# Performance work log

Measured on AMD Instinct MI355X. Metric: run time of the kernel, lower is better.

Reference implementation:

```python
import jax, jax.numpy as jnp
import numpy as np

EPS = 1e-12  # torch F.normalize eps

def _normalize(x):
    # L2-normalize along last dim, matching F.normalize(dim=-1)
    n = jnp.linalg.norm(x, axis=-1, keepdims=True)
    return x / jnp.maximum(n, EPS)

def setup_inputs() -> dict:
    key = jax.random.key(0)
    k1, k2, k3 = jax.random.split(key, 3)
    B, K, D = 32768, 8, 256
    return {
        "drone_slots": jax.random.normal(k1, (B, K, D), dtype=jnp.float32),
        "sat_slots": jax.random.normal(k2, (B, K, D), dtype=jnp.float32),
        "labels": jax.random.randint(k3, (B,), 0, 1000, dtype=jnp.int64),
        "temperature": 0.1,
    }

def reference(drone_slots, sat_slots, labels, temperature):
    # labels are unused by the original math (targets are arange(K))
    ds = _normalize(drone_slots)  # [B,K,D]
    ss = _normalize(sat_slots)    # [B,K,D]
    logits = jnp.einsum("bkd,bjd->bkj", ds, ss) / temperature  # [B,K,K]
    # cross_entropy with targets = arange(K): positive is the diagonal
    lse = jax.nn.logsumexp(logits, axis=-1)                      # [B,K]
    pos = jnp.diagonal(logits, axis1=-2, axis2=-1)               # [B,K]
    ce_per_sample = jnp.mean(lse - pos, axis=-1)                 # [B], per-sample mean-reduced CE
    return jnp.mean(ce_per_sample)                               # average over batch
```

## Files before the change

kernel.cpp:

```cpp
#include <hip/hip_runtime.h>


#define GSTAGE(P, NH) do {                                              \
    const unsigned bp = (lane >> (P)) & 1u;                             \
    _Pragma("unroll")                                                   \
    for (int c = 0; c < (NH); ++c) {                                    \
      float keep = bp ? g[(NH) + c] : g[c];                             \
      float send = bp ? g[c] : g[(NH) + c];                             \
      g[c] = keep + __shfl_xor(send, 1 << (P), 64);                     \
    }                                                                   \
  } while (0)

#define NSTAGE(arr, LB, NH, MASK) do {                                  \
    const unsigned bp = (lane >> (LB)) & 1u;                            \
    _Pragma("unroll")                                                   \
    for (int c = 0; c < (NH); ++c) {                                    \
      float keep = bp ? arr[(NH) + c] : arr[c];                         \
      float send = bp ? arr[c] : arr[(NH) + c];                         \
      arr[c] = keep + __shfl_xor(send, (MASK), 64);                     \
    }                                                                   \
  } while (0)

extern "C" __global__ __launch_bounds__(256, 2)
void slot_ce_main(const float* __restrict__ ds, const float* __restrict__ ss,
                  const float* __restrict__ tptr, float* __restrict__ ws,
                  int B, int nwaves) {
  const int tid  = blockIdx.x * blockDim.x + threadIdx.x;
  const int wave = tid >> 6;
  const int lane = threadIdx.x & 63;
  const float inv_t = 1.0f / tptr[0];

  float acc = 0.0f;

  for (int b = wave; b < B; b += nwaves) {
    const float4* av = (const float4*)(ds + (size_t)b * 2048);
    const float4* sv = (const float4*)(ss + (size_t)b * 2048);
    float4 A[8], S[8];
#pragma unroll
    for (int k = 0; k < 8; ++k) {
      A[k] = av[k * 64 + lane];
      S[k] = sv[k * 64 + lane];
    }

    float g[64];
#pragma unroll
    for (int k = 0; k < 8; ++k)
#pragma unroll
      for (int j = 0; j < 8; ++j)
        g[k * 8 + j] = A[k].x * S[j].x + A[k].y * S[j].y +
                       A[k].z * S[j].z + A[k].w * S[j].w;

    float na[8], nb[8];
#pragma unroll
    for (int k = 0; k < 8; ++k) {
      na[k] = A[k].x * A[k].x + A[k].y * A[k].y + A[k].z * A[k].z + A[k].w * A[k].w;
      nb[k] = S[k].x * S[k].x + S[k].y * S[k].y + S[k].z * S[k].z + S[k].w * S[k].w;
    }

    GSTAGE(5, 32); GSTAGE(4, 16); GSTAGE(3, 8);
    GSTAGE(2, 4);  GSTAGE(1, 2);  GSTAGE(0, 1);

    NSTAGE(na, 5, 4, 32); NSTAGE(na, 4, 2, 16); NSTAGE(na, 3, 1, 8);
    na[0] += __shfl_xor(na[0], 4, 64);
    na[0] += __shfl_xor(na[0], 2, 64);
    na[0] += __shfl_xor(na[0], 1, 64);
    NSTAGE(nb, 2, 4, 4); NSTAGE(nb, 1, 2, 2); NSTAGE(nb, 0, 1, 1);
    nb[0] += __shfl_xor(nb[0], 32, 64);
    nb[0] += __shfl_xor(nb[0], 16, 64);
    nb[0] += __shfl_xor(nb[0],  8, 64);

    float logit = g[0] * rsqrtf(na[0] * nb[0]) * inv_t;

    float m = logit;
    m = fmaxf(m, __shfl_xor(m, 1, 64));
    m = fmaxf(m, __shfl_xor(m, 2, 64));
    m = fmaxf(m, __shfl_xor(m, 4, 64));
    float e = __expf(logit - m);
    e += __shfl_xor(e, 1, 64);
    e += __shfl_xor(e, 2, 64);
    e += __shfl_xor(e, 4, 64);
    float lse = m + __logf(e);

    acc += lse * 0.125f;
    if ((lane >> 3) == (lane & 7)) acc -= logit;
  }

  __shared__ float red[4];
#pragma unroll
  for (int o = 32; o >= 1; o >>= 1) acc += __shfl_xor(acc, o, 64);
  if (lane == 0) red[threadIdx.x >> 6] = acc;
  __syncthreads();
  if (threadIdx.x == 0)
    ws[blockIdx.x] = (red[0] + red[1]) + (red[2] + red[3]);
}

extern "C" __global__ __launch_bounds__(256)
void slot_ce_finish(const float* __restrict__ ws, float* __restrict__ out,
                    int nparts, float scale) {
  __shared__ float red[256];
  float s = 0.0f;
  for (int i = threadIdx.x; i < nparts; i += 256) s += ws[i];
  red[threadIdx.x] = s;
  __syncthreads();
  for (int o = 128; o >= 1; o >>= 1) {
    if ((int)threadIdx.x < o) red[threadIdx.x] += red[threadIdx.x + o];
    __syncthreads();
  }
  if (threadIdx.x == 0) out[0] = red[0] * scale;
}

extern "C" void kernel_launch(void* const* d_in, const int* in_sizes, int n_in,
                              void* d_out, int out_size, void* d_ws, size_t ws_size,
                              hipStream_t stream) {
  const float* ds   = (const float*)d_in[0];
  const float* ss   = (const float*)d_in[1];
  const float* tptr = (const float*)d_in[3];
  float* out = (float*)d_out;
  float* ws  = (float*)d_ws;

  const int B = in_sizes[0] / (8 * 256);
  const int blocks = 2048;
  const int nwaves = blocks * (256 / 64);

  slot_ce_main<<<blocks, 256, 0, stream>>>(ds, ss, tptr, ws, B, nwaves);
  const float scale = 1.0f / (8.0f * (float)B);
  slot_ce_finish<<<1, 256, 0, stream>>>(ws, out, blocks, scale);
}
```

Before: 99.38 us.

## Compute slot similarity with bf16 MFMA over two-sample tiles per wave

Replaces the per-sample FP32 dot products and butterfly shuffle reductions with a 16x16x32 bf16 MFMA. Each wave handles two batch samples (16 rows) at once and keeps only the diagonal 8x8 blocks of the result. Launch changes from a persistent grid-stride loop to one tile per wave. The inputs are converted to bf16 for the matmul while the norms stay in FP32, which loses precision and needs extra conversion ALU work. The kernel also assumes B is even.

```diff
diff --git a/kernel.cpp b/kernel.cpp
--- a/kernel.cpp
+++ b/kernel.cpp
@@ -1,94 +1,91 @@
 #include <hip/hip_runtime.h>
 
 
-#define GSTAGE(P, NH) do {                                              \
-    const unsigned bp = (lane >> (P)) & 1u;                             \
-    _Pragma("unroll")                                                   \
-    for (int c = 0; c < (NH); ++c) {                                    \
-      float keep = bp ? g[(NH) + c] : g[c];                             \
-      float send = bp ? g[c] : g[(NH) + c];                             \
-      g[c] = keep + __shfl_xor(send, 1 << (P), 64);                     \
-    }                                                                   \
-  } while (0)
+typedef __attribute__((ext_vector_type(8))) short bf16x8;
+typedef __attribute__((ext_vector_type(4))) float f32x4;
 
-#define NSTAGE(arr, LB, NH, MASK) do {                                  \
-    const unsigned bp = (lane >> (LB)) & 1u;                            \
-    _Pragma("unroll")                                                   \
-    for (int c = 0; c < (NH); ++c) {                                    \
-      float keep = bp ? arr[(NH) + c] : arr[c];                         \
-      float send = bp ? arr[c] : arr[(NH) + c];                         \
-      arr[c] = keep + __shfl_xor(send, (MASK), 64);                     \
-    }                                                                   \
-  } while (0)
+__device__ inline short f2bf(float f) {
+  union { float f; unsigned u; } v; v.f = f;
+  unsigned u = v.u;
+  u += 0x7fffu + ((u >> 16) & 1u);
+  return (short)(u >> 16);
+}
 
-extern "C" __global__ __launch_bounds__(256, 2)
-void slot_ce_main(const float* __restrict__ ds, const float* __restrict__ ss,
+extern "C" __global__ __launch_bounds__(256)
+void slot_ce_mfma(const float* __restrict__ ds, const float* __restrict__ ss,
                   const float* __restrict__ tptr, float* __restrict__ ws,
-                  int B, int nwaves) {
-  const int tid  = blockIdx.x * blockDim.x + threadIdx.x;
-  const int wave = tid >> 6;
+                  int ntiles) {
   const int lane = threadIdx.x & 63;
+  const int wid  = (blockIdx.x * (blockDim.x >> 6)) + (threadIdx.x >> 6);
+  const int m = lane & 15;
+  const int h = lane >> 4;
   const float inv_t = 1.0f / tptr[0];
 
-  float acc = 0.0f;
+  float loss = 0.0f;
 
-  for (int b = wave; b < B; b += nwaves) {
-    const float4* av = (const float4*)(ds + (size_t)b * 2048);
-    const float4* sv = (const float4*)(ss + (size_t)b * 2048);
-    float4 A[8], S[8];
+  if (wid < ntiles) {
+    const float4* pa = (const float4*)(ds + (size_t)wid * 4096);
+    const float4* pb = (const float4*)(ss + (size_t)wid * 4096);
+    const int base = m * 64 + h * 2;
+
+    f32x4 acc = {0.f, 0.f, 0.f, 0.f};
+    float ssqA = 0.f, ssqS = 0.f;
+
 #pragma unroll
-    for (int k = 0; k < 8; ++k) {
-      A[k] = av[k * 64 + lane];
-      S[k] = sv[k * 64 + lane];
+    for (int kb = 0; kb < 8; ++kb) {
+      const int idx = base + kb * 8;
+      float4 a0 = pa[idx], a1 = pa[idx + 1];
+      float4 s0 = pb[idx], s1 = pb[idx + 1];
+
+      ssqA += a0.x*a0.x + a0.y*a0.y + a0.z*a0.z + a0.w*a0.w
+            + a1.x*a1.x + a1.y*a1.y + a1.z*a1.z + a1.w*a1.w;
+      ssqS += s0.x*s0.x + s0.y*s0.y + s0.z*s0.z + s0.w*s0.w
+            + s1.x*s1.x + s1.y*s1.y + s1.z*s1.z + s1.w*s1.w;
+
+      bf16x8 af = { f2bf(a0.x), f2bf(a0.y), f2bf(a0.z), f2bf(a0.w),
+                    f2bf(a1.x), f2bf(a1.y), f2bf(a1.z), f2bf(a1.w) };
+      bf16x8 sf = { f2bf(s0.x), f2bf(s0.y), f2bf(s0.z), f2bf(s0.w),
+                    f2bf(s1.x), f2bf(s1.y), f2bf(s1.z), f2bf(s1.w) };
+      acc = __builtin_amdgcn_mfma_f32_16x16x32_bf16(af, sf, acc, 0, 0, 0);
     }
 
-    float g[64];
+    ssqA += __shfl_xor(ssqA, 16, 64);
+    ssqA += __shfl_xor(ssqA, 32, 64);
+    ssqS += __shfl_xor(ssqS, 16, 64);
+    ssqS += __shfl_xor(ssqS, 32, 64);
+    float na0 = __shfl(ssqA, h * 4 + 0, 64);
+    float na1 = __shfl(ssqA, h * 4 + 1, 64);
+    float na2 = __shfl(ssqA, h * 4 + 2, 64);
+    float na3 = __shfl(ssqA, h * 4 + 3, 64);
+
+    float lg0 = acc[0] * rsqrtf(na0 * ssqS) * inv_t;
+    float lg1 = acc[1] * rsqrtf(na1 * ssqS) * inv_t;
+    float lg2 = acc[2] * rsqrtf(na2 * ssqS) * inv_t;
+    float lg3 = acc[3] * rsqrtf(na3 * ssqS) * inv_t;
+
+    float c = 0.0f;
 #pragma unroll
-    for (int k = 0; k < 8; ++k)
-#pragma unroll
-      for (int j = 0; j < 8; ++j)
-        g[k * 8 + j] = A[k].x * S[j].x + A[k].y * S[j].y +
-                       A[k].z * S[j].z + A[k].w * S[j].w;
-
-    float na[8], nb[8];
-#pragma unroll
-    for (int k = 0; k < 8; ++k) {
-      na[k] = A[k].x * A[k].x + A[k].y * A[k].y + A[k].z * A[k].z + A[k].w * A[k].w;
-      nb[k] = S[k].x * S[k].x + S[k].y * S[k].y + S[k].z * S[k].z + S[k].w * S[k].w;
+    for (int r = 0; r < 4; ++r) {
+      float lg = r == 0 ? lg0 : r == 1 ? lg1 : r == 2 ? lg2 : lg3;
+      float mx = lg;
+      mx = fmaxf(mx, __shfl_xor(mx, 1, 64));
+      mx = fmaxf(mx, __shfl_xor(mx, 2, 64));
+      mx = fmaxf(mx, __shfl_xor(mx, 4, 64));
+      float e = __expf(lg - mx);
+      e += __shfl_xor(e, 1, 64);
+      e += __shfl_xor(e, 2, 64);
+      e += __shfl_xor(e, 4, 64);
+      float lse = mx + __logf(e);
+      c += lse * 0.125f;
+      if (4 * h + r == m) c -= lg;
     }
-
-    GSTAGE(5, 32); GSTAGE(4, 16); GSTAGE(3, 8);
-    GSTAGE(2, 4);  GSTAGE(1, 2);  GSTAGE(0, 1);
-
-    NSTAGE(na, 5, 4, 32); NSTAGE(na, 4, 2, 16); NSTAGE(na, 3, 1, 8);
-    na[0] += __shfl_xor(na[0], 4, 64);
-    na[0] += __shfl_xor(na[0], 2, 64);
-    na[0] += __shfl_xor(na[0], 1, 64);
-    NSTAGE(nb, 2, 4, 4); NSTAGE(nb, 1, 2, 2); NSTAGE(nb, 0, 1, 1);
-    nb[0] += __shfl_xor(nb[0], 32, 64);
-    nb[0] += __shfl_xor(nb[0], 16, 64);
-    nb[0] += __shfl_xor(nb[0],  8, 64);
-
-    float logit = g[0] * rsqrtf(na[0] * nb[0]) * inv_t;
-
-    float m = logit;
-    m = fmaxf(m, __shfl_xor(m, 1, 64));
-    m = fmaxf(m, __shfl_xor(m, 2, 64));
-    m = fmaxf(m, __shfl_xor(m, 4, 64));
-    float e = __expf(logit - m);
-    e += __shfl_xor(e, 1, 64);
-    e += __shfl_xor(e, 2, 64);
-    e += __shfl_xor(e, 4, 64);
-    float lse = m + __logf(e);
-
-    acc += lse * 0.125f;
-    if ((lane >> 3) == (lane & 7)) acc -= logit;
+    if ((m >= 8) == (h >= 2)) loss = c;
   }
 
+#pragma unroll
+  for (int o = 32; o >= 1; o >>= 1) loss += __shfl_xor(loss, o, 64);
   __shared__ float red[4];
-#pragma unroll
-  for (int o = 32; o >= 1; o >>= 1) acc += __shfl_xor(acc, o, 64);
-  if (lane == 0) red[threadIdx.x >> 6] = acc;
+  if (lane == 0) red[threadIdx.x >> 6] = loss;
   __syncthreads();
   if (threadIdx.x == 0)
     ws[blockIdx.x] = (red[0] + red[1]) + (red[2] + red[3]);
@@ -118,11 +115,11 @@
   float* out = (float*)d_out;
   float* ws  = (float*)d_ws;
 
-  const int B = in_sizes[0] / (8 * 256);
-  const int blocks = 2048;
-  const int nwaves = blocks * (256 / 64);
+  const int B      = in_sizes[0] / (8 * 256);
+  const int ntiles = B / 2;
+  const int blocks = (ntiles + 3) / 4;
 
-  slot_ce_main<<<blocks, 256, 0, stream>>>(ds, ss, tptr, ws, B, nwaves);
+  slot_ce_mfma<<<blocks, 256, 0, stream>>>(ds, ss, tptr, ws, ntiles);
   const float scale = 1.0f / (8.0f * (float)B);
   slot_ce_finish<<<1, 256, 0, stream>>>(ws, out, blocks, scale);
 }
```

Result: slower. 106.6 us (+7.2%).
